# Kernel optimization log

Hardware: AMD Instinct MI355X
Metric: run time of the kernel (lower is better)

Reference implementation:

```python
import jax, jax.numpy as jnp
import numpy as np

N, DIM, HEADS, DHEAD = 4096, 1024, 16, 64
INNER = HEADS * DHEAD


def setup_inputs() -> dict:
    key = jax.random.key(0)
    ks = jax.random.split(key, 6)
    s_in = 1.0 / np.sqrt(DIM)
    s_inner = 1.0 / np.sqrt(INNER)
    return {
        "x": jax.random.normal(ks[0], (N, DIM), dtype=jnp.float32),
        # weights stored as (in, out) so y = x @ W
        "Wq": jax.random.uniform(ks[1], (DIM, INNER), jnp.float32, -s_in, s_in),
        "Wk": jax.random.uniform(ks[2], (DIM, INNER), jnp.float32, -s_in, s_in),
        "Wv": jax.random.uniform(ks[3], (DIM, INNER), jnp.float32, -s_in, s_in),
        "Wo": jax.random.uniform(ks[4], (INNER, DIM), jnp.float32, -s_inner, s_inner),
        "bo": jax.random.uniform(ks[5], (DIM,), jnp.float32, -s_inner, s_inner),
    }


def reference(x, Wq, Wk, Wv, Wo, bo):
    scale = DHEAD ** -0.5
    # [n, h, d] -> [h, n, d]
    q = (x @ Wq).reshape(N, HEADS, DHEAD).transpose(1, 0, 2)
    k = (x @ Wk).reshape(N, HEADS, DHEAD).transpose(1, 0, 2)
    v = (x @ Wv).reshape(N, HEADS, DHEAD).transpose(1, 0, 2)
    dots = jnp.einsum("hnd,hmd->hnm", q, k) * scale  # [h, n, n]
    attn = jax.nn.softmax(dots, axis=-1)
    out = jnp.einsum("hnm,hmd->hnd", attn, v)  # [h, n, d]
    out = out.transpose(1, 0, 2).reshape(N, INNER)
    return out @ Wo + bo
```

## Files before the change

### kernel.cpp

```cpp
#include <hip/hip_runtime.h>
#include <cstdint>
#include <cstddef>

typedef _Float16 f16;
typedef _Float16 f16x8 __attribute__((ext_vector_type(8)));
typedef _Float16 f16x4 __attribute__((ext_vector_type(4)));
typedef __fp16 fp16x2 __attribute__((ext_vector_type(2)));
typedef float floatx4 __attribute__((ext_vector_type(4)));
typedef float floatx16 __attribute__((ext_vector_type(16)));

constexpr int SEQ = 4096;
constexpr int DIM = 1024;
constexpr int NHEAD = 16;
constexpr int DH = 64;

#define QSCALE 0.18033688011112042f

__device__ __forceinline__ void async16(void* lds, const void* g) {
  __builtin_amdgcn_global_load_lds(
      (__attribute__((address_space(1))) void*)g,
      (__attribute__((address_space(3))) void*)lds, 16, 0, 0);
}

__device__ __forceinline__ uint32_t pk2(float a, float b) {
  union { fp16x2 h; uint32_t u; } c;
  c.h = __builtin_amdgcn_cvt_pkrtz(a, b);
  return c.u;
}

__device__ __forceinline__ float dot2acc(uint32_t packed, float acc) {
#if __has_builtin(__builtin_amdgcn_fdot2)
  union { uint32_t u; fp16x2 h; } c; c.u = packed;
  fp16x2 one2; one2.x = (__fp16)1.0f; one2.y = (__fp16)1.0f;
  return __builtin_amdgcn_fdot2(c.h, one2, acc, false);
#else
  union { uint32_t u; fp16x2 h; } c; c.u = packed;
  return acc + (float)c.h.x + (float)c.h.y;
#endif
}

__global__ void prep(const float* __restrict__ x, const float* __restrict__ w0,
                     const float* __restrict__ w1, const float* __restrict__ w2,
                     const float* __restrict__ w3, f16* __restrict__ xh,
                     f16* __restrict__ o0, f16* __restrict__ o1,
                     f16* __restrict__ o2, f16* __restrict__ o3) {
  int z = blockIdx.z;
  if (z == 4) {
    int blk = blockIdx.y * 32 + blockIdx.x;
    int tid = threadIdx.y * 32 + threadIdx.x;
    int base = (blk * 256 + tid) * 4;
#pragma unroll
    for (int c = 0; c < 4; ++c) {
      int i = base + c * (SEQ * DIM / 4);
      float4 v = *(const float4*)(x + i);
      f16x4 o;
      o.x = (f16)v.x; o.y = (f16)v.y; o.z = (f16)v.z; o.w = (f16)v.w;
      *(f16x4*)(xh + i) = o;
    }
    return;
  }
  __shared__ float tile[32][33];
  const float* W = (z == 0) ? w0 : (z == 1) ? w1 : (z == 2) ? w2 : w3;
  f16* O = (z == 0) ? o0 : (z == 1) ? o1 : (z == 2) ? o2 : o3;
  int tx = threadIdx.x, ty = threadIdx.y;
  int xc = blockIdx.x * 32 + tx;
  for (int i = ty; i < 32; i += 8)
    tile[i][tx] = W[(size_t)(blockIdx.y * 32 + i) * DIM + xc];
  __syncthreads();
  int xo = blockIdx.y * 32 + tx;
  for (int i = ty; i < 32; i += 8)
    O[(size_t)(blockIdx.x * 32 + i) * DIM + xo] = (f16)tile[tx][i];
}

__global__ __launch_bounds__(256, 2) void gemm_qkv(
    const f16* __restrict__ xh, const f16* __restrict__ wqt,
    const f16* __restrict__ wkt, const f16* __restrict__ wvt,
    f16* __restrict__ q_ws, f16* __restrict__ k_ws, f16* __restrict__ vt_ws) {
  __shared__ f16 smem[24576];
  const int tid = threadIdx.x;
  const int lane = tid & 63, l16 = lane & 15, quad = lane >> 4;
  const int w = tid >> 6, wr = w >> 1, wc = w & 1;
  const int m0 = blockIdx.x * 128, n0 = blockIdx.y * 256;
  const int z = blockIdx.z;
  const f16* Bt = (z == 0) ? wqt : (z == 1) ? wkt : wvt;

  floatx4 acc[4][8];
#pragma unroll
  for (int mt = 0; mt < 4; ++mt)
#pragma unroll
    for (int nt = 0; nt < 8; ++nt) acc[mt][nt] = (floatx4){0.f, 0.f, 0.f, 0.f};

#define QKV_STAGE(t_, buf_)                                                    \
  {                                                                            \
    int k0_ = (t_) * 32;                                                       \
    _Pragma("unroll")                                                          \
    for (int rnd = 0; rnd < 2; ++rnd) {                                        \
      int e = (rnd * 256 + tid) * 8;                                           \
      int cb = e >> 10, r = (e >> 3) & 127;                                    \
      async16((buf_) + e, xh + (size_t)(m0 + r) * DIM + k0_ + cb * 8);         \
    }                                                                          \
    _Pragma("unroll")                                                          \
    for (int rnd = 0; rnd < 4; ++rnd) {                                        \
      int e = (rnd * 256 + tid) * 8;                                           \
      int cb = e >> 11, r = (e >> 3) & 255;                                    \
      async16((buf_) + 4096 + e, Bt + (size_t)(n0 + r) * DIM + k0_ + cb * 8);  \
    }                                                                          \
  }

  QKV_STAGE(0, smem);
  for (int t = 0; t < 32; ++t) {
    f16* cur = smem + (t & 1) * 12288;
    if (t + 1 < 32) {
      QKV_STAGE(t + 1, smem + ((t + 1) & 1) * 12288);
      asm volatile("s_waitcnt vmcnt(6)" ::: "memory");
    } else {
      asm volatile("s_waitcnt vmcnt(0)" ::: "memory");
    }
    __builtin_amdgcn_s_barrier();
    asm volatile("" ::: "memory");
    const f16* a_lds = cur;
    const f16* b_lds = cur + 4096;
    f16x8 af[4], bq[8];
#pragma unroll
    for (int mt = 0; mt < 4; ++mt)
      af[mt] = *(const f16x8*)(a_lds + quad * 1024 + (wr * 64 + mt * 16 + l16) * 8);
#pragma unroll
    for (int nt = 0; nt < 8; ++nt)
      bq[nt] = *(const f16x8*)(b_lds + quad * 2048 + (wc * 128 + nt * 16 + l16) * 8);
#pragma unroll
    for (int mt = 0; mt < 4; ++mt)
#pragma unroll
      for (int nt = 0; nt < 8; ++nt)
        acc[mt][nt] = __builtin_amdgcn_mfma_f32_16x16x32_f16(af[mt], bq[nt], acc[mt][nt], 0, 0, 0);
    asm volatile("" ::: "memory");
    __builtin_amdgcn_s_barrier();
  }
#undef QKV_STAGE

  if (z < 2) {
#pragma unroll
    for (int mt = 0; mt < 4; ++mt)
#pragma unroll
      for (int nt = 0; nt < 8; ++nt)
#pragma unroll
        for (int r = 0; r < 4; ++r) {
          int m = m0 + wr * 64 + mt * 16 + quad * 4 + r;
          int c = n0 + wc * 128 + nt * 16 + l16;
          float v = acc[mt][nt][r];
          if (z == 0)
            q_ws[(size_t)((c >> 6) * SEQ + m) * DH + (c & 63)] = (f16)(v * QSCALE);
          else
            k_ws[(size_t)((c >> 6) * SEQ + m) * DH + (c & 63)] = (f16)v;
        }
  } else {
#pragma unroll
    for (int ch = 0; ch < 2; ++ch) {
      if (wc == ch) {
#pragma unroll
        for (int mt = 0; mt < 4; ++mt)
#pragma unroll
          for (int nt = 0; nt < 8; ++nt)
#pragma unroll
            for (int r = 0; r < 4; ++r) {
              int cl = nt * 16 + l16;
              int ml = wr * 64 + mt * 16 + quad * 4 + r;
              smem[cl * 132 + ml] = (f16)acc[mt][nt][r];
            }
      }
      __syncthreads();
#pragma unroll
      for (int it = 0; it < 8; ++it) {
        int idx = it * 256 + tid;
        int cl = idx >> 4, mp = (idx & 15) * 8;
        f16x4 lo = *(const f16x4*)(smem + cl * 132 + mp);
        f16x4 hi4 = *(const f16x4*)(smem + cl * 132 + mp + 4);
        f16x8 v8;
#pragma unroll
        for (int j = 0; j < 4; ++j) { v8[j] = lo[j]; v8[4 + j] = hi4[j]; }
        *(f16x8*)(vt_ws + (size_t)(n0 + ch * 128 + cl) * SEQ + m0 + mp) = v8;
      }
      __syncthreads();
    }
  }
}

__global__ __launch_bounds__(256, 4) void attn_kernel(
    const f16* __restrict__ qg, const f16* __restrict__ kg,
    const f16* __restrict__ vtg, f16* __restrict__ og) {
  __shared__ f16 smem[16384];

  const int tid = threadIdx.x;
  const int w = tid >> 6, lane = tid & 63, l32 = lane & 31;
  const int hi = lane >> 5;

  const int pid = blockIdx.x + 32 * blockIdx.y;
  const int vid = (pid & 7) * 64 + (pid >> 3);
  const int qt = vid & 31, h = vid >> 5;

  const int q0 = qt * 128 + w * 32;

  f16x8 qf[4];
#pragma unroll
  for (int kf = 0; kf < 4; ++kf)
    qf[kf] = *(const f16x8*)(qg + (size_t)(h * SEQ + q0 + l32) * DH + kf * 16 + hi * 8);

  floatx16 oacc[2];
  oacc[0] = (floatx16)0.f; oacc[1] = (floatx16)0.f;
  float ssa = 0.f, ssb = 0.f;

  const f16* kg_h = kg + (size_t)h * SEQ * DH;
  const f16* vt_h = vtg + (size_t)h * DH * SEQ;
  constexpr int NT = SEQ / 64;

  {
#pragma unroll
    for (int rnd = 0; rnd < 2; ++rnd) {
      int e = (rnd * 256 + tid) * 8;
      int cb = e >> 9, r = (e >> 3) & 63;
      async16(smem + e, kg_h + (size_t)r * DH + cb * 8);
      async16(smem + 4096 + e, vt_h + (size_t)r * SEQ + cb * 8);
    }
  }

  for (int i = 0; i < NT; ++i) {
    f16* k_lds = smem + (i & 1) * 8192;
    f16* v_lds = k_lds + 4096;
    if (i + 1 < NT) {
      f16* kn = smem + ((i + 1) & 1) * 8192;
      const f16* ks = kg_h + (size_t)((i + 1) * 64) * DH;
      const f16* vs = vt_h + (i + 1) * 64;
#pragma unroll
      for (int rnd = 0; rnd < 2; ++rnd) {
        int e = (rnd * 256 + tid) * 8;
        int cb = e >> 9, r = (e >> 3) & 63;
        async16(kn + e, ks + (size_t)r * DH + cb * 8);
        async16(kn + 4096 + e, vs + (size_t)r * SEQ + cb * 8);
      }
      asm volatile("s_waitcnt vmcnt(4)" ::: "memory");
    } else {
      asm volatile("s_waitcnt vmcnt(0)" ::: "memory");
    }
    __builtin_amdgcn_s_barrier();
    asm volatile("" ::: "memory");

    floatx16 s0 = (floatx16)0.f, s1 = (floatx16)0.f;
    __builtin_amdgcn_s_setprio(1);
#pragma unroll
    for (int kf = 0; kf < 4; ++kf) {
      const f16* kr = k_lds + (kf * 2 + hi) * 512;
      f16x8 ka = *(const f16x8*)(kr + l32 * 8);
      f16x8 kc = *(const f16x8*)(kr + (32 + l32) * 8);
      s0 = __builtin_amdgcn_mfma_f32_32x32x16_f16(ka, qf[kf], s0, 0, 0, 0);
      s1 = __builtin_amdgcn_mfma_f32_32x32x16_f16(kc, qf[kf], s1, 0, 0, 0);
    }
    __builtin_amdgcn_s_setprio(0);

#pragma unroll
    for (int kb = 0; kb < 2; ++kb) {
      const floatx16 sacc = kb ? s1 : s0;
      f16x8 vf[2][2];
#pragma unroll
      for (int kh = 0; kh < 2; ++kh) {
        int cb = kb * 4 + kh * 2 + hi;
#pragma unroll
        for (int dt = 0; dt < 2; ++dt)
          vf[kh][dt] = *(const f16x8*)(v_lds + cb * 512 + (dt * 32 + l32) * 8);
      }
      float p[16];
#pragma unroll
      for (int r = 0; r < 16; ++r) p[r] = __builtin_amdgcn_exp2f(sacc[r]);
#pragma unroll
      for (int kh = 0; kh < 2; ++kh) {
        uint32_t d0a = pk2(p[8 * kh + 0], p[8 * kh + 1]);
        uint32_t d0b = pk2(p[8 * kh + 2], p[8 * kh + 3]);
        uint32_t d1a = pk2(p[8 * kh + 4], p[8 * kh + 5]);
        uint32_t d1b = pk2(p[8 * kh + 6], p[8 * kh + 7]);
        ssa = dot2acc(d0a, ssa);
        ssa = dot2acc(d0b, ssa);
        ssb = dot2acc(d1a, ssb);
        ssb = dot2acc(d1b, ssb);
        union { uint32_t u[4]; f16x8 v; } bu;
#if __has_builtin(__builtin_amdgcn_permlane32_swap)
        {
          auto sw1 = __builtin_amdgcn_permlane32_swap(d0a, d1a, false, false);
          auto sw2 = __builtin_amdgcn_permlane32_swap(d0b, d1b, false, false);
          bu.u[0] = sw1[0]; bu.u[1] = sw2[0]; bu.u[2] = sw1[1]; bu.u[3] = sw2[1];
        }
#else
        {
          uint32_t ra = (uint32_t)__shfl_xor((int)(hi ? d0a : d1a), 32);
          uint32_t rb = (uint32_t)__shfl_xor((int)(hi ? d0b : d1b), 32);
          bu.u[0] = hi ? ra : d0a;
          bu.u[1] = hi ? rb : d0b;
          bu.u[2] = hi ? d1a : ra;
          bu.u[3] = hi ? d1b : rb;
        }
#endif
        __builtin_amdgcn_s_setprio(1);
#pragma unroll
        for (int dt = 0; dt < 2; ++dt)
          oacc[dt] = __builtin_amdgcn_mfma_f32_32x32x16_f16(vf[kh][dt], bu.v, oacc[dt], 0, 0, 0);
        __builtin_amdgcn_s_setprio(0);
      }
    }
    asm volatile("" ::: "memory");
    __builtin_amdgcn_s_barrier();
    asm volatile("" ::: "memory");
  }

  float ssum = ssa + ssb;
  ssum += __shfl_xor(ssum, 32);
  float rn = 1.f / ssum;

  __syncthreads();
  f16* t = smem;
  const int ql = w * 32 + l32;
#pragma unroll
  for (int dt = 0; dt < 2; ++dt)
#pragma unroll
    for (int g = 0; g < 4; ++g) {
      f16x4 v4;
#pragma unroll
      for (int j = 0; j < 4; ++j) v4[j] = (f16)(oacc[dt][g * 4 + j] * rn);
      *(f16x4*)(t + ql * 68 + dt * 32 + 8 * g + 4 * hi) = v4;
    }
  __syncthreads();
#pragma unroll
  for (int it = 0; it < 4; ++it) {
    int idx = it * 256 + tid;
    int q = idx >> 3, dcol = (idx & 7) * 8;
    f16x4 lo = *(const f16x4*)(t + q * 68 + dcol);
    f16x4 hi4 = *(const f16x4*)(t + q * 68 + dcol + 4);
    f16x8 v8;
#pragma unroll
    for (int j = 0; j < 4; ++j) { v8[j] = lo[j]; v8[4 + j] = hi4[j]; }
    *(f16x8*)(og + (size_t)(qt * 128 + q) * DIM + h * DH + dcol) = v8;
  }
}

__global__ __launch_bounds__(512, 2) void gemm_o(
    const f16* __restrict__ ab, const f16* __restrict__ wot,
    const float* __restrict__ bo, float* __restrict__ out) {
  __shared__ f16 smem[16384];
  const int tid = threadIdx.x;
  const int lane = tid & 63, l16 = lane & 15, quad = lane >> 4;
  const int w = tid >> 6, wr = w >> 2, wc = w & 3;
  const int m0 = blockIdx.x * 128, n0 = blockIdx.y * 128;

  floatx4 acc[4][2];
#pragma unroll
  for (int mt = 0; mt < 4; ++mt)
#pragma unroll
    for (int nt = 0; nt < 2; ++nt) acc[mt][nt] = (floatx4){0.f, 0.f, 0.f, 0.f};

#define O_STAGE(t_, buf_)                                                      \
  {                                                                            \
    int k0_ = (t_) * 32;                                                       \
    int e = tid * 8;                                                           \
    int cb = e >> 10, r = (e >> 3) & 127;                                      \
    async16((buf_) + e, ab + (size_t)(m0 + r) * DIM + k0_ + cb * 8);           \
    async16((buf_) + 4096 + e, wot + (size_t)(n0 + r) * DIM + k0_ + cb * 8);   \
  }

  O_STAGE(0, smem);
  for (int t = 0; t < 32; ++t) {
    f16* cur = smem + (t & 1) * 8192;
    if (t + 1 < 32) {
      O_STAGE(t + 1, smem + ((t + 1) & 1) * 8192);
      asm volatile("s_waitcnt vmcnt(2)" ::: "memory");
    } else {
      asm volatile("s_waitcnt vmcnt(0)" ::: "memory");
    }
    __builtin_amdgcn_s_barrier();
    asm volatile("" ::: "memory");
    const f16* a_lds = cur;
    const f16* b_lds = cur + 4096;
    f16x8 af[4], bq[2];
#pragma unroll
    for (int mt = 0; mt < 4; ++mt)
      af[mt] = *(const f16x8*)(a_lds + quad * 1024 + (wr * 64 + mt * 16 + l16) * 8);
#pragma unroll
    for (int nt = 0; nt < 2; ++nt)
      bq[nt] = *(const f16x8*)(b_lds + quad * 1024 + (wc * 32 + nt * 16 + l16) * 8);
#pragma unroll
    for (int mt = 0; mt < 4; ++mt)
#pragma unroll
      for (int nt = 0; nt < 2; ++nt)
        acc[mt][nt] = __builtin_amdgcn_mfma_f32_16x16x32_f16(af[mt], bq[nt], acc[mt][nt], 0, 0, 0);
    asm volatile("" ::: "memory");
    __builtin_amdgcn_s_barrier();
  }
#undef O_STAGE

#pragma unroll
  for (int mt = 0; mt < 4; ++mt)
#pragma unroll
    for (int nt = 0; nt < 2; ++nt)
#pragma unroll
      for (int r = 0; r < 4; ++r) {
        int m = m0 + wr * 64 + mt * 16 + quad * 4 + r;
        int c = n0 + wc * 32 + nt * 16 + l16;
        out[(size_t)m * DIM + c] = acc[mt][nt][r] + bo[c];
      }
}


extern "C" void kernel_launch(void* const* d_in, const int* in_sizes, int n_in,
                              void* d_out, int out_size, void* d_ws, size_t ws_size,
                              hipStream_t stream) {
  (void)in_sizes; (void)n_in; (void)out_size; (void)ws_size;
  const float* x  = (const float*)d_in[0];
  const float* Wq = (const float*)d_in[1];
  const float* Wk = (const float*)d_in[2];
  const float* Wv = (const float*)d_in[3];
  const float* Wo = (const float*)d_in[4];
  const float* bo = (const float*)d_in[5];
  float* out = (float*)d_out;
  char* ws = (char*)d_ws;

  f16* xh    = (f16*)(ws);
  f16* wqt   = (f16*)(ws + (8u  << 20));
  f16* wkt   = (f16*)(ws + (10u << 20));
  f16* wvt   = (f16*)(ws + (12u << 20));
  f16* wot   = (f16*)(ws + (14u << 20));
  f16* q_ws  = (f16*)(ws + (16u << 20));
  f16* k_ws  = (f16*)(ws + (24u << 20));
  f16* vt_ws = (f16*)(ws + (32u << 20));
  f16* aout  = xh;

  prep<<<dim3(32, 32, 5), dim3(32, 8), 0, stream>>>(x, Wq, Wk, Wv, Wo, xh, wqt, wkt, wvt, wot);
  gemm_qkv<<<dim3(32, 4, 3), dim3(256), 0, stream>>>(xh, wqt, wkt, wvt, q_ws, k_ws, vt_ws);
  attn_kernel<<<dim3(SEQ / 128, NHEAD), dim3(256), 0, stream>>>(q_ws, k_ws, vt_ws, aout);
  gemm_o<<<dim3(32, 8), dim3(512), 0, stream>>>(aout, wot, bo, out);
}
```

Baseline: 241.6 us.

## Remap GEMM block IDs per XCD, stage Q/K stores via LDS, raise occupancy

Block IDs in the QKV and output-projection GEMMs are remapped so that blocks landing on the same XCD (round-robin by pid mod 8) cover contiguous tiles, aiming to improve L2 reuse of shared A/B panels. Q and K epilogue stores are staged through LDS and written as 16-byte vectors instead of scattered 2-byte stores. The QKV kernel's launch bounds are raised to 3 blocks per CU, which may force register spilling given the 128 fp32 accumulators per thread.

```diff
diff --git a/kernel.cpp b/kernel.cpp
--- a/kernel.cpp
+++ b/kernel.cpp
@@ -72,7 +72,7 @@
     O[(size_t)(blockIdx.x * 32 + i) * DIM + xo] = (f16)tile[tx][i];
 }
 
-__global__ __launch_bounds__(256, 2) void gemm_qkv(
+__global__ __launch_bounds__(256, 3) void gemm_qkv(
     const f16* __restrict__ xh, const f16* __restrict__ wqt,
     const f16* __restrict__ wkt, const f16* __restrict__ wvt,
     f16* __restrict__ q_ws, f16* __restrict__ k_ws, f16* __restrict__ vt_ws) {
@@ -80,8 +80,11 @@
   const int tid = threadIdx.x;
   const int lane = tid & 63, l16 = lane & 15, quad = lane >> 4;
   const int w = tid >> 6, wr = w >> 1, wc = w & 1;
-  const int m0 = blockIdx.x * 128, n0 = blockIdx.y * 256;
-  const int z = blockIdx.z;
+  const int pid = blockIdx.x + 32 * (blockIdx.y + 4 * blockIdx.z);
+  const int vid = (pid & 7) * 48 + (pid >> 3);
+  const int bx = vid & 31, g = vid >> 5;
+  const int by = g & 3, z = g >> 2;
+  const int m0 = bx * 128, n0 = by * 256;
   const f16* Bt = (z == 0) ? wqt : (z == 1) ? wkt : wvt;
 
   floatx4 acc[4][8];
@@ -138,20 +141,37 @@
 #undef QKV_STAGE
 
   if (z < 2) {
-#pragma unroll
-    for (int mt = 0; mt < 4; ++mt)
-#pragma unroll
-      for (int nt = 0; nt < 8; ++nt)
-#pragma unroll
-        for (int r = 0; r < 4; ++r) {
-          int m = m0 + wr * 64 + mt * 16 + quad * 4 + r;
-          int c = n0 + wc * 128 + nt * 16 + l16;
-          float v = acc[mt][nt][r];
-          if (z == 0)
-            q_ws[(size_t)((c >> 6) * SEQ + m) * DH + (c & 63)] = (f16)(v * QSCALE);
-          else
-            k_ws[(size_t)((c >> 6) * SEQ + m) * DH + (c & 63)] = (f16)v;
-        }
+    f16* dst = (z == 0) ? q_ws : k_ws;
+#pragma unroll
+    for (int ch = 0; ch < 2; ++ch) {
+      if (wc == ch) {
+#pragma unroll
+        for (int mt = 0; mt < 4; ++mt)
+#pragma unroll
+          for (int nt = 0; nt < 8; ++nt)
+#pragma unroll
+            for (int r = 0; r < 4; ++r) {
+              int ml = wr * 64 + mt * 16 + quad * 4 + r;
+              int cl = nt * 16 + l16;
+              float v = acc[mt][nt][r];
+              smem[ml * 132 + cl] = (f16)((z == 0) ? v * QSCALE : v);
+            }
+      }
+      __syncthreads();
+#pragma unroll
+      for (int it = 0; it < 8; ++it) {
+        int idx = it * 256 + tid;
+        int m = idx >> 4, cc = (idx & 15) * 8;
+        f16x4 lo = *(const f16x4*)(smem + m * 132 + cc);
+        f16x4 hi4 = *(const f16x4*)(smem + m * 132 + cc + 4);
+        f16x8 v8;
+#pragma unroll
+        for (int j = 0; j < 4; ++j) { v8[j] = lo[j]; v8[4 + j] = hi4[j]; }
+        int c = n0 + ch * 128 + cc;
+        *(f16x8*)(dst + (size_t)((c >> 6) * SEQ + m0 + m) * DH + (c & 63)) = v8;
+      }
+      __syncthreads();
+    }
   } else {
 #pragma unroll
     for (int ch = 0; ch < 2; ++ch) {
@@ -345,7 +365,9 @@
   const int tid = threadIdx.x;
   const int lane = tid & 63, l16 = lane & 15, quad = lane >> 4;
   const int w = tid >> 6, wr = w >> 2, wc = w & 3;
-  const int m0 = blockIdx.x * 128, n0 = blockIdx.y * 128;
+  const int pid = blockIdx.x + 32 * blockIdx.y;
+  const int vid = (pid & 7) * 32 + (pid >> 3);
+  const int m0 = (vid & 31) * 128, n0 = (vid >> 5) * 128;
 
   floatx4 acc[4][2];
 #pragma unroll
```

Result: slower. 297.1 us (+23.0%).
